# Performance work log

Hardware: AMD Instinct MI355X
Metric: run time of the kernel (lower is better)

The kernel has to match this reference:

```python
import jax, jax.numpy as jnp
import numpy as np

NUM_HEADS = 12
D = 768
HD = D // NUM_HEADS  # 64

def setup_inputs() -> dict:
    key = jax.random.key(0)
    ks = jax.random.split(key, 9)
    s = 0.02
    return {
        "x": jax.random.normal(ks[0], (4, 2048, D), dtype=jnp.float32),
        "QW_w": jax.random.normal(ks[1], (D, D), dtype=jnp.float32) * s,
        "QW_b": jax.random.normal(ks[2], (D,), dtype=jnp.float32) * s,
        "KW_w": jax.random.normal(ks[3], (D, D), dtype=jnp.float32) * s,
        "KW_b": jax.random.normal(ks[4], (D,), dtype=jnp.float32) * s,
        "VW_w": jax.random.normal(ks[5], (D, D), dtype=jnp.float32) * s,
        "VW_b": jax.random.normal(ks[6], (D,), dtype=jnp.float32) * s,
        "OW_w": jax.random.normal(ks[7], (D, D), dtype=jnp.float32) * s,
        "OW_b": jax.random.normal(ks[8], (D,), dtype=jnp.float32) * s,
    }

def reference(x, QW_w, QW_b, KW_w, KW_b, VW_w, VW_b, OW_w, OW_b):
    b, s, _ = x.shape
    # torch nn.Linear: y = x @ W.T + b
    def proj(w, bias):
        y = jnp.einsum('bsd,ed->bse', x, w) + bias
        return y.reshape(b, s, NUM_HEADS, HD).transpose(0, 2, 1, 3)  # [b,h,s,hd]
    q = proj(QW_w, QW_b)
    k = proj(KW_w, KW_b)
    v = proj(VW_w, VW_b)
    scores = jnp.einsum('bhqd,bhkd->bhqk', q, k) / jnp.sqrt(jnp.float32(HD))
    attn = jax.nn.softmax(scores, axis=-1)
    out = jnp.einsum('bhqk,bhkd->bhqd', attn, v)
    out = out.transpose(0, 2, 1, 3).reshape(b, s, NUM_HEADS * HD)
    return jnp.einsum('bsd,ed->bse', out, OW_w) + OW_b
```

## Files before the change

### kernel.cpp

```cpp
#include <hip/hip_runtime.h>
#include <hip/hip_bf16.h>

#define NH  12
#define HD  64
#define DIM 768
#define SEQ 2048
#define NB  4
#define MM  (NB*SEQ)
#define NKB (SEQ/64)

typedef short    v8s  __attribute__((ext_vector_type(8)));
typedef float    v4f  __attribute__((ext_vector_type(4)));
typedef float    v16f __attribute__((ext_vector_type(16)));
typedef unsigned v4u  __attribute__((ext_vector_type(4)));

#if __has_builtin(__builtin_amdgcn_exp2f)
#define EXP2(x) __builtin_amdgcn_exp2f(x)
#else
#define EXP2(x) __builtin_exp2f(x)
#endif

static __device__ __forceinline__ unsigned short f2b(float f) {
    unsigned int u = __float_as_uint(f);
    return (unsigned short)((u + 0x7FFFu + ((u >> 16) & 1u)) >> 16);
}
static __device__ __forceinline__ unsigned pk2bf(float lo, float hi) {
    return __builtin_amdgcn_perm(__float_as_uint(hi) + 0x8000u,
                                 __float_as_uint(lo) + 0x8000u, 0x07060302u);
}
static __device__ __forceinline__ void g2l16(const unsigned short* g, unsigned short* l) {
    __builtin_amdgcn_global_load_lds(
        (const __attribute__((address_space(1))) void*)g,
        (__attribute__((address_space(3))) void*)l, 16, 0, 0);
}

__global__ void cast_f32_bf16(const float* __restrict__ in,
                              unsigned short* __restrict__ out, int n4) {
    int i = blockIdx.x * blockDim.x + threadIdx.x;
    if (i < n4) {
        float4 v = reinterpret_cast<const float4*>(in)[i];
        ushort4 o;
        o.x = f2b(v.x); o.y = f2b(v.y); o.z = f2b(v.z); o.w = f2b(v.w);
        reinterpret_cast<ushort4*>(out)[i] = o;
    }
}

__global__ void cast4_f32_bf16(const float* __restrict__ i0, const float* __restrict__ i1,
                               const float* __restrict__ i2, const float* __restrict__ i3,
                               unsigned short* __restrict__ o0, unsigned short* __restrict__ o1,
                               unsigned short* __restrict__ o2, unsigned short* __restrict__ o3,
                               int n4) {
    int i = blockIdx.x * blockDim.x + threadIdx.x;
    if (i >= n4) return;
    const float* in; unsigned short* out;
    switch (blockIdx.y) {
        case 0: in = i0; out = o0; break;
        case 1: in = i1; out = o1; break;
        case 2: in = i2; out = o2; break;
        default: in = i3; out = o3; break;
    }
    float4 v = reinterpret_cast<const float4*>(in)[i];
    ushort4 o;
    o.x = f2b(v.x); o.y = f2b(v.y); o.z = f2b(v.z); o.w = f2b(v.w);
    reinterpret_cast<ushort4*>(out)[i] = o;
}

__global__ __launch_bounds__(256, 3) void gemm_qkv(
    const unsigned short* __restrict__ A,
    const unsigned short* __restrict__ Wq,
    const unsigned short* __restrict__ Wk,
    const unsigned short* __restrict__ Wv,
    const float* __restrict__ bq,
    const float* __restrict__ bk,
    const float* __restrict__ bvp,
    unsigned short* __restrict__ Qb,
    unsigned short* __restrict__ Kb,
    unsigned short* __restrict__ Vf)
{
    __shared__ __align__(16) unsigned short As[128 * 64];
    __shared__ __align__(16) unsigned short Bs[3][64 * 64];

    const int tid  = threadIdx.x;
    const int w    = tid >> 6, lane = tid & 63;
    const int quad = lane >> 4, l16 = lane & 15;
    const int wm   = w & 1,  wn = w >> 1;
    const int lane8 = lane >> 3, sc = lane & 7;
    const int m0   = blockIdx.x * 128;
    const int h    = blockIdx.y;
    const int n0   = h * 64;

    v4f acc[3][4][2];
    #pragma unroll
    for (int s = 0; s < 3; ++s)
        #pragma unroll
        for (int i = 0; i < 4; ++i)
            #pragma unroll
            for (int j = 0; j < 2; ++j)
                acc[s][i][j] = v4f{0.f, 0.f, 0.f, 0.f};

    for (int kb = 0; kb < DIM; kb += 64) {
        __syncthreads();
        #pragma unroll
        for (int t = 0; t < 4; ++t) {
            int r8 = w * 32 + t * 8;
            int r  = r8 + lane8;
            int gch = sc ^ (r & 7);
            g2l16(&A[(size_t)(m0 + r) * DIM + kb + gch * 8], &As[r8 * 64]);
        }
        #pragma unroll
        for (int u = 0; u < 6; ++u) {
            int G = w * 6 + u;
            int set = G >> 3, rg = G & 7;
            int row = rg * 8 + lane8;
            int gch = sc ^ (row & 7);
            const unsigned short* Wp = (set == 0) ? Wq : (set == 1) ? Wk : Wv;
            g2l16(&Wp[(size_t)(n0 + row) * DIM + kb + gch * 8], &Bs[set][rg * 8 * 64]);
        }
        __syncthreads();
        #pragma unroll
        for (int kk = 0; kk < 64; kk += 32) {
            int chb = kk >> 3;
            v8s a[4];
            #pragma unroll
            for (int i = 0; i < 4; ++i) {
                int m = wm * 64 + i * 16 + l16;
                a[i] = *reinterpret_cast<const v8s*>(
                    &As[m * 64 + (((chb + quad) ^ (m & 7)) << 3)]);
            }
            #pragma unroll
            for (int s = 0; s < 3; ++s) {
                v8s b[2];
                #pragma unroll
                for (int j = 0; j < 2; ++j) {
                    int n = wn * 32 + j * 16 + l16;
                    b[j] = *reinterpret_cast<const v8s*>(
                        &Bs[s][n * 64 + (((chb + quad) ^ (n & 7)) << 3)]);
                }
                #pragma unroll
                for (int i = 0; i < 4; ++i)
                    #pragma unroll
                    for (int j = 0; j < 2; ++j)
                        acc[s][i][j] = __builtin_amdgcn_mfma_f32_16x16x32_bf16(
                            a[i], b[j], acc[s][i][j], 0, 0, 0);
            }
        }
    }

    #pragma unroll
    for (int s = 0; s < 2; ++s) {
        unsigned short* out = s ? Kb : Qb;
        const float* bias   = s ? bk : bq;
        const float scale   = s ? 1.0f : 0.1803368801f;
        #pragma unroll
        for (int i = 0; i < 4; ++i) {
            #pragma unroll
            for (int j = 0; j < 2; ++j) {
                int hd = wn * 32 + j * 16 + l16;
                float bias_v = bias[n0 + hd];
                #pragma unroll
                for (int r = 0; r < 4; ++r) {
                    int gm = m0 + wm * 64 + i * 16 + quad * 4 + r;
                    int bb = gm >> 11, sq = gm & (SEQ - 1);
                    out[((size_t)(bb * NH + h) * SEQ + sq) * HD + hd] =
                        f2b((acc[s][i][j][r] + bias_v) * scale);
                }
            }
        }
    }
    #pragma unroll
    for (int i = 0; i < 4; ++i) {
        #pragma unroll
        for (int j = 0; j < 2; ++j) {
            int hd = wn * 32 + j * 16 + l16;
            int hb = hd >> 5, l31v = hd & 31;
            float bias_v = bvp[n0 + hd];
            int gm0 = m0 + wm * 64 + i * 16 + quad * 4;
            int bb = gm0 >> 11, sk = gm0 & (SEQ - 1);
            int kbi = sk >> 6;
            int halfv = quad >> 1, j0 = (quad & 1) * 4;
            ushort4 pkv;
            pkv.x = f2b(acc[2][i][j][0] + bias_v);
            pkv.y = f2b(acc[2][i][j][1] + bias_v);
            pkv.z = f2b(acc[2][i][j][2] + bias_v);
            pkv.w = f2b(acc[2][i][j][3] + bias_v);
            size_t frag = ((size_t)(bb * NH + h) * NKB + kbi) * 8 + hb * 4 + i;
            *reinterpret_cast<ushort4*>(
                &Vf[frag * 512 + (halfv * 32 + l31v) * 8 + j0]) = pkv;
        }
    }
}

__global__ __launch_bounds__(256) void gemm_o(
    const unsigned short* __restrict__ A,
    const unsigned short* __restrict__ W,
    const float* __restrict__ bias,
    float* __restrict__ out)
{
    __shared__ __align__(16) unsigned short As[128 * 64];
    __shared__ __align__(16) unsigned short Bs[128 * 64];

    const int tid  = threadIdx.x;
    const int w    = tid >> 6, lane = tid & 63;
    const int quad = lane >> 4, l16 = lane & 15;
    const int wm   = w & 1,  wn = w >> 1;
    const int lane8 = lane >> 3, sc = lane & 7;
    const int m0  = blockIdx.x * 128;
    const int n0l = blockIdx.y * 128;

    v4f acc[4][4];
    #pragma unroll
    for (int i = 0; i < 4; ++i)
        #pragma unroll
        for (int j = 0; j < 4; ++j)
            acc[i][j] = v4f{0.f, 0.f, 0.f, 0.f};

    for (int kb = 0; kb < DIM; kb += 64) {
        __syncthreads();
        #pragma unroll
        for (int t = 0; t < 4; ++t) {
            int r8 = w * 32 + t * 8;
            int r  = r8 + lane8;
            int gch = sc ^ (r & 7);
            g2l16(&A[(size_t)(m0  + r) * DIM + kb + gch * 8], &As[r8 * 64]);
            g2l16(&W[(size_t)(n0l + r) * DIM + kb + gch * 8], &Bs[r8 * 64]);
        }
        __syncthreads();
        #pragma unroll
        for (int kk = 0; kk < 64; kk += 32) {
            v8s a[4], b[4];
            int chb = kk >> 3;
            #pragma unroll
            for (int i = 0; i < 4; ++i) {
                int m = wm * 64 + i * 16 + l16;
                a[i] = *reinterpret_cast<const v8s*>(
                    &As[m * 64 + (((chb + quad) ^ (m & 7)) << 3)]);
                int n = wn * 64 + i * 16 + l16;
                b[i] = *reinterpret_cast<const v8s*>(
                    &Bs[n * 64 + (((chb + quad) ^ (n & 7)) << 3)]);
            }
            #pragma unroll
            for (int i = 0; i < 4; ++i)
                #pragma unroll
                for (int j = 0; j < 4; ++j)
                    acc[i][j] = __builtin_amdgcn_mfma_f32_16x16x32_bf16(a[i], b[j], acc[i][j], 0, 0, 0);
        }
    }

    #pragma unroll
    for (int i = 0; i < 4; ++i) {
        #pragma unroll
        for (int j = 0; j < 4; ++j) {
            int gn = n0l + wn * 64 + j * 16 + l16;
            float bias_v = bias[gn];
            #pragma unroll
            for (int r = 0; r < 4; ++r) {
                int gm = m0 + wm * 64 + i * 16 + quad * 4 + r;
                out[(size_t)gm * DIM + gn] = acc[i][j][r] + bias_v;
            }
        }
    }
}

__global__ __launch_bounds__(256, 3) void attn(
    const unsigned short* __restrict__ Q,
    const unsigned short* __restrict__ K,
    const unsigned short* __restrict__ Vf,
    unsigned short* __restrict__ ctx)
{
    __shared__ __align__(16) unsigned short Ks[2][64 * 64];

    const int tid  = threadIdx.x;
    const int w    = tid >> 6, lane = tid & 63;
    const int l31  = lane & 31, half = lane >> 5;
    const int lane8 = lane >> 3, sc = lane & 7;
    const int bh   = blockIdx.y;
    const int b    = bh / NH, h = bh % NH;
    const int q0   = blockIdx.x * 128 + w * 32;

    const unsigned short* Qp = Q  + ((size_t)bh * SEQ + q0) * HD;
    const unsigned short* Kp = K  + (size_t)bh * SEQ * HD;
    const unsigned short* Vh = Vf + (size_t)bh * NKB * 8 * 512 + lane * 8;

    v8s bq[4];
    #pragma unroll
    for (int c = 0; c < 4; ++c)
        bq[c] = *reinterpret_cast<const v8s*>(&Qp[l31 * HD + c * 16 + half * 8]);

    v8s va[2][4], vb[2][4];
    #pragma unroll
    for (int hb = 0; hb < 2; ++hb)
        #pragma unroll
        for (int c = 0; c < 4; ++c)
            va[hb][c] = *reinterpret_cast<const v8s*>(&Vh[(hb * 4 + c) * 512]);

    v16f o0, o1, Z;
    #pragma unroll
    for (int i = 0; i < 16; ++i) { o0[i] = 0.f; o1[i] = 0.f; Z[i] = 0.f; }
    float li = 0.f;

    const int rx = l31 & 7;
    int rdoff[4];
    #pragma unroll
    for (int c = 0; c < 4; ++c)
        rdoff[c] = l31 * 64 + (((c * 2 + half) ^ rx) << 3);

    #define STAGE_K(kb_, buf_)                                                       \
        do {                                                                         \
            _Pragma("unroll")                                                        \
            for (int t = 0; t < 2; ++t) {                                            \
                int r8  = (t * 4 + w) * 8;                                           \
                int row = r8 + lane8;                                                \
                int gch = sc ^ (row & 7);                                            \
                g2l16(&Kp[(size_t)((kb_) + row) * HD + gch * 8], &Ks[buf_][r8 * 64]);\
            }                                                                        \
        } while (0)

    #define TILE(IT, BUF, VCUR, VNEXT)                                               \
    {                                                                                \
        __syncthreads();                                                             \
        if ((IT) + 1 < NKB) {                                                        \
            STAGE_K(((IT) + 1) * 64, (BUF) ^ 1);                                     \
            const unsigned short* Vn = Vh + (size_t)((IT) + 1) * 8 * 512;            \
            _Pragma("unroll")                                                        \
            for (int hb = 0; hb < 2; ++hb)                                           \
                _Pragma("unroll")                                                    \
                for (int c = 0; c < 4; ++c)                                          \
                    VNEXT[hb][c] = *reinterpret_cast<const v8s*>(&Vn[(hb*4+c)*512]); \
        }                                                                            \
        v16f s0, s1;                                                                 \
        {                                                                            \
            v8s ka0 = *reinterpret_cast<const v8s*>(&Ks[BUF][rdoff[0]]);             \
            v8s ka1 = *reinterpret_cast<const v8s*>(&Ks[BUF][rdoff[0] + 2048]);      \
            s0 = __builtin_amdgcn_mfma_f32_32x32x16_bf16(ka0, bq[0], Z, 0, 0, 0);    \
            s1 = __builtin_amdgcn_mfma_f32_32x32x16_bf16(ka1, bq[0], Z, 0, 0, 0);    \
            _Pragma("unroll")                                                        \
            for (int c = 1; c < 4; ++c) {                                            \
                v8s k0 = *reinterpret_cast<const v8s*>(&Ks[BUF][rdoff[c]]);          \
                v8s k1 = *reinterpret_cast<const v8s*>(&Ks[BUF][rdoff[c] + 2048]);   \
                s0 = __builtin_amdgcn_mfma_f32_32x32x16_bf16(k0, bq[c], s0, 0, 0, 0);\
                s1 = __builtin_amdgcn_mfma_f32_32x32x16_bf16(k1, bq[c], s1, 0, 0, 0);\
            }                                                                        \
        }                                                                            \
        unsigned pk[8][2];                                                           \
        _Pragma("unroll")                                                            \
        for (int g = 0; g < 4; ++g) {                                                \
            float e0 = EXP2(s0[4*g+0]), e1 = EXP2(s0[4*g+1]);                        \
            float e2 = EXP2(s0[4*g+2]), e3 = EXP2(s0[4*g+3]);                        \
            li += (e0 + e1) + (e2 + e3);                                             \
            pk[g][0] = pk2bf(e0, e1);                                                \
            pk[g][1] = pk2bf(e2, e3);                                                \
            float f0 = EXP2(s1[4*g+0]), f1 = EXP2(s1[4*g+1]);                        \
            float f2 = EXP2(s1[4*g+2]), f3 = EXP2(s1[4*g+3]);                        \
            li += (f0 + f1) + (f2 + f3);                                             \
            pk[4+g][0] = pk2bf(f0, f1);                                              \
            pk[4+g][1] = pk2bf(f2, f3);                                              \
        }                                                                            \
        _Pragma("unroll")                                                            \
        for (int cp = 0; cp < 4; ++cp) {                                             \
            unsigned a0 = pk[2*cp][0],   a1 = pk[2*cp][1];                           \
            unsigned b0 = pk[2*cp+1][0], b1 = pk[2*cp+1][1];                         \
            unsigned u0 = half ? a0 : b0;                                            \
            unsigned u1 = half ? a1 : b1;                                            \
            unsigned x0 = __shfl_xor(u0, 32);                                        \
            unsigned x1 = __shfl_xor(u1, 32);                                        \
            v4u fw;                                                                  \
            fw.x = half ? x0 : a0;                                                   \
            fw.y = half ? x1 : a1;                                                   \
            fw.z = half ? b0 : x0;                                                   \
            fw.w = half ? b1 : x1;                                                   \
            v8s pf = __builtin_bit_cast(v8s, fw);                                    \
            o0 = __builtin_amdgcn_mfma_f32_32x32x16_bf16(VCUR[0][cp], pf, o0, 0,0,0);\
            o1 = __builtin_amdgcn_mfma_f32_32x32x16_bf16(VCUR[1][cp], pf, o1, 0,0,0);\
        }                                                                            \
    }

    STAGE_K(0, 0);

    for (int it = 0; it < NKB; it += 2) {
        TILE(it,     0, va, vb)
        TILE(it + 1, 1, vb, va)
    }
    #undef TILE
    #undef STAGE_K

    float inv = 1.0f / (li + __shfl_xor(li, 32));

    const int q = q0 + l31;
    size_t base = ((size_t)(b * SEQ + q)) * DIM + h * HD;
    #pragma unroll
    for (int g = 0; g < 4; ++g) {
        int hd0 = 8 * g + 4 * half;
        uint2 u0, u1;
        u0.x = pk2bf(o0[4*g+0] * inv, o0[4*g+1] * inv);
        u0.y = pk2bf(o0[4*g+2] * inv, o0[4*g+3] * inv);
        u1.x = pk2bf(o1[4*g+0] * inv, o1[4*g+1] * inv);
        u1.y = pk2bf(o1[4*g+2] * inv, o1[4*g+3] * inv);
        *reinterpret_cast<uint2*>(&ctx[base + hd0])      = u0;
        *reinterpret_cast<uint2*>(&ctx[base + 32 + hd0]) = u1;
    }
}

extern "C" void kernel_launch(void* const* d_in, const int* in_sizes, int n_in,
                              void* d_out, int out_size, void* d_ws, size_t ws_size,
                              hipStream_t stream) {
    const float* x  = (const float*)d_in[0];
    const float* qw = (const float*)d_in[1]; const float* qb = (const float*)d_in[2];
    const float* kw = (const float*)d_in[3]; const float* kb = (const float*)d_in[4];
    const float* vw = (const float*)d_in[5]; const float* vb = (const float*)d_in[6];
    const float* ow = (const float*)d_in[7]; const float* ob = (const float*)d_in[8];
    float* out = (float*)d_out;

    char* ws = (char*)d_ws;
    size_t off = 0;
    auto alloc = [&](size_t bytes) -> unsigned short* {
        unsigned short* p = (unsigned short*)(ws + off);
        off += (bytes + 255) & ~(size_t)255;
        return p;
    };
    const size_t XB = (size_t)MM * DIM * 2;
    const size_t WB = (size_t)DIM * DIM * 2;
    const size_t QB = (size_t)NB * NH * SEQ * HD * 2;

    unsigned short* xb  = alloc(XB);
    unsigned short* wqb = alloc(WB);
    unsigned short* wkb = alloc(WB);
    unsigned short* wvb = alloc(WB);
    unsigned short* wob = alloc(WB);
    unsigned short* Qb  = alloc(QB);
    unsigned short* Kb  = alloc(QB);
    unsigned short* Vfb = alloc(QB);
    unsigned short* ctx = alloc(XB);

    const int n4x = MM * DIM / 4;
    const int n4w = DIM * DIM / 4;
    cast_f32_bf16<<<(n4x + 255) / 256, 256, 0, stream>>>(x, xb, n4x);
    cast4_f32_bf16<<<dim3((n4w + 255) / 256, 4), 256, 0, stream>>>(
        qw, kw, vw, ow, wqb, wkb, wvb, wob, n4w);

    gemm_qkv<<<dim3(MM / 128, NH), 256, 0, stream>>>(
        xb, wqb, wkb, wvb, qb, kb, vb, Qb, Kb, Vfb);

    attn<<<dim3(SEQ / 128, NB * NH), 256, 0, stream>>>(Qb, Kb, Vfb, ctx);

    gemm_o<<<dim3(MM / 128, DIM / 128), 256, 0, stream>>>(ctx, wob, ob, out);
}
```

Measured before the change: 228.7 us.

## Shrink output GEMM N-tile and single-buffer V fragments in attention

```diff
diff --git a/kernel.cpp b/kernel.cpp
--- a/kernel.cpp
+++ b/kernel.cpp
@@ -190,14 +190,14 @@
     }
 }
 
-__global__ __launch_bounds__(256) void gemm_o(
+__global__ __launch_bounds__(256, 3) void gemm_o(
     const unsigned short* __restrict__ A,
     const unsigned short* __restrict__ W,
     const float* __restrict__ bias,
     float* __restrict__ out)
 {
     __shared__ __align__(16) unsigned short As[128 * 64];
-    __shared__ __align__(16) unsigned short Bs[128 * 64];
+    __shared__ __align__(16) unsigned short Bs[64 * 64];
 
     const int tid  = threadIdx.x;
     const int w    = tid >> 6, lane = tid & 63;
@@ -205,13 +205,13 @@
     const int wm   = w & 1,  wn = w >> 1;
     const int lane8 = lane >> 3, sc = lane & 7;
     const int m0  = blockIdx.x * 128;
-    const int n0l = blockIdx.y * 128;
-
-    v4f acc[4][4];
+    const int n0l = blockIdx.y * 64;
+
+    v4f acc[4][2];
     #pragma unroll
     for (int i = 0; i < 4; ++i)
         #pragma unroll
-        for (int j = 0; j < 4; ++j)
+        for (int j = 0; j < 2; ++j)
             acc[i][j] = v4f{0.f, 0.f, 0.f, 0.f};
 
     for (int kb = 0; kb < DIM; kb += 64) {
@@ -221,27 +221,36 @@
             int r8 = w * 32 + t * 8;
             int r  = r8 + lane8;
             int gch = sc ^ (r & 7);
-            g2l16(&A[(size_t)(m0  + r) * DIM + kb + gch * 8], &As[r8 * 64]);
+            g2l16(&A[(size_t)(m0 + r) * DIM + kb + gch * 8], &As[r8 * 64]);
+        }
+        #pragma unroll
+        for (int t = 0; t < 2; ++t) {
+            int r8 = (w * 2 + t) * 8;
+            int r  = r8 + lane8;
+            int gch = sc ^ (r & 7);
             g2l16(&W[(size_t)(n0l + r) * DIM + kb + gch * 8], &Bs[r8 * 64]);
         }
         __syncthreads();
         #pragma unroll
         for (int kk = 0; kk < 64; kk += 32) {
-            v8s a[4], b[4];
+            v8s a[4], b[2];
             int chb = kk >> 3;
             #pragma unroll
             for (int i = 0; i < 4; ++i) {
                 int m = wm * 64 + i * 16 + l16;
                 a[i] = *reinterpret_cast<const v8s*>(
                     &As[m * 64 + (((chb + quad) ^ (m & 7)) << 3)]);
-                int n = wn * 64 + i * 16 + l16;
-                b[i] = *reinterpret_cast<const v8s*>(
+            }
+            #pragma unroll
+            for (int j = 0; j < 2; ++j) {
+                int n = wn * 32 + j * 16 + l16;
+                b[j] = *reinterpret_cast<const v8s*>(
                     &Bs[n * 64 + (((chb + quad) ^ (n & 7)) << 3)]);
             }
             #pragma unroll
             for (int i = 0; i < 4; ++i)
                 #pragma unroll
-                for (int j = 0; j < 4; ++j)
+                for (int j = 0; j < 2; ++j)
                     acc[i][j] = __builtin_amdgcn_mfma_f32_16x16x32_bf16(a[i], b[j], acc[i][j], 0, 0, 0);
         }
     }
@@ -249,8 +258,8 @@
     #pragma unroll
     for (int i = 0; i < 4; ++i) {
         #pragma unroll
-        for (int j = 0; j < 4; ++j) {
-            int gn = n0l + wn * 64 + j * 16 + l16;
+        for (int j = 0; j < 2; ++j) {
+            int gn = n0l + wn * 32 + j * 16 + l16;
             float bias_v = bias[gn];
             #pragma unroll
             for (int r = 0; r < 4; ++r) {
@@ -286,7 +295,7 @@
     for (int c = 0; c < 4; ++c)
         bq[c] = *reinterpret_cast<const v8s*>(&Qp[l31 * HD + c * 16 + half * 8]);
 
-    v8s va[2][4], vb[2][4];
+    v8s va[2][4];
     #pragma unroll
     for (int hb = 0; hb < 2; ++hb)
         #pragma unroll
@@ -315,72 +324,70 @@
             }                                                                        \
         } while (0)
 
-    #define TILE(IT, BUF, VCUR, VNEXT)                                               \
-    {                                                                                \
-        __syncthreads();                                                             \
-        if ((IT) + 1 < NKB) {                                                        \
-            STAGE_K(((IT) + 1) * 64, (BUF) ^ 1);                                     \
-            const unsigned short* Vn = Vh + (size_t)((IT) + 1) * 8 * 512;            \
-            _Pragma("unroll")                                                        \
-            for (int hb = 0; hb < 2; ++hb)                                           \
-                _Pragma("unroll")                                                    \
-                for (int c = 0; c < 4; ++c)                                          \
-                    VNEXT[hb][c] = *reinterpret_cast<const v8s*>(&Vn[(hb*4+c)*512]); \
-        }                                                                            \
-        v16f s0, s1;                                                                 \
-        {                                                                            \
-            v8s ka0 = *reinterpret_cast<const v8s*>(&Ks[BUF][rdoff[0]]);             \
-            v8s ka1 = *reinterpret_cast<const v8s*>(&Ks[BUF][rdoff[0] + 2048]);      \
-            s0 = __builtin_amdgcn_mfma_f32_32x32x16_bf16(ka0, bq[0], Z, 0, 0, 0);    \
-            s1 = __builtin_amdgcn_mfma_f32_32x32x16_bf16(ka1, bq[0], Z, 0, 0, 0);    \
-            _Pragma("unroll")                                                        \
-            for (int c = 1; c < 4; ++c) {                                            \
-                v8s k0 = *reinterpret_cast<const v8s*>(&Ks[BUF][rdoff[c]]);          \
-                v8s k1 = *reinterpret_cast<const v8s*>(&Ks[BUF][rdoff[c] + 2048]);   \
-                s0 = __builtin_amdgcn_mfma_f32_32x32x16_bf16(k0, bq[c], s0, 0, 0, 0);\
-                s1 = __builtin_amdgcn_mfma_f32_32x32x16_bf16(k1, bq[c], s1, 0, 0, 0);\
-            }                                                                        \
-        }                                                                            \
-        unsigned pk[8][2];                                                           \
-        _Pragma("unroll")                                                            \
-        for (int g = 0; g < 4; ++g) {                                                \
-            float e0 = EXP2(s0[4*g+0]), e1 = EXP2(s0[4*g+1]);                        \
-            float e2 = EXP2(s0[4*g+2]), e3 = EXP2(s0[4*g+3]);                        \
-            li += (e0 + e1) + (e2 + e3);                                             \
-            pk[g][0] = pk2bf(e0, e1);                                                \
-            pk[g][1] = pk2bf(e2, e3);                                                \
-            float f0 = EXP2(s1[4*g+0]), f1 = EXP2(s1[4*g+1]);                        \
-            float f2 = EXP2(s1[4*g+2]), f3 = EXP2(s1[4*g+3]);                        \
-            li += (f0 + f1) + (f2 + f3);                                             \
-            pk[4+g][0] = pk2bf(f0, f1);                                              \
-            pk[4+g][1] = pk2bf(f2, f3);                                              \
-        }                                                                            \
-        _Pragma("unroll")                                                            \
-        for (int cp = 0; cp < 4; ++cp) {                                             \
-            unsigned a0 = pk[2*cp][0],   a1 = pk[2*cp][1];                           \
-            unsigned b0 = pk[2*cp+1][0], b1 = pk[2*cp+1][1];                         \
-            unsigned u0 = half ? a0 : b0;                                            \
-            unsigned u1 = half ? a1 : b1;                                            \
-            unsigned x0 = __shfl_xor(u0, 32);                                        \
-            unsigned x1 = __shfl_xor(u1, 32);                                        \
-            v4u fw;                                                                  \
-            fw.x = half ? x0 : a0;                                                   \
-            fw.y = half ? x1 : a1;                                                   \
-            fw.z = half ? b0 : x0;                                                   \
-            fw.w = half ? b1 : x1;                                                   \
-            v8s pf = __builtin_bit_cast(v8s, fw);                                    \
-            o0 = __builtin_amdgcn_mfma_f32_32x32x16_bf16(VCUR[0][cp], pf, o0, 0,0,0);\
-            o1 = __builtin_amdgcn_mfma_f32_32x32x16_bf16(VCUR[1][cp], pf, o1, 0,0,0);\
-        }                                                                            \
-    }
-
     STAGE_K(0, 0);
 
-    for (int it = 0; it < NKB; it += 2) {
-        TILE(it,     0, va, vb)
-        TILE(it + 1, 1, vb, va)
-    }
-    #undef TILE
+    for (int it = 0; it < NKB; ++it) {
+        const int buf = it & 1;
+        __syncthreads();
+        if (it + 1 < NKB) STAGE_K((it + 1) * 64, buf ^ 1);
+
+        v16f s0, s1;
+        {
+            v8s ka00 = *reinterpret_cast<const v8s*>(&Ks[buf][rdoff[0]]);
+            v8s ka10 = *reinterpret_cast<const v8s*>(&Ks[buf][rdoff[0] + 2048]);
+            s0 = __builtin_amdgcn_mfma_f32_32x32x16_bf16(ka00, bq[0], Z, 0, 0, 0);
+            s1 = __builtin_amdgcn_mfma_f32_32x32x16_bf16(ka10, bq[0], Z, 0, 0, 0);
+            #pragma unroll
+            for (int c = 1; c < 4; ++c) {
+                v8s k0 = *reinterpret_cast<const v8s*>(&Ks[buf][rdoff[c]]);
+                v8s k1 = *reinterpret_cast<const v8s*>(&Ks[buf][rdoff[c] + 2048]);
+                s0 = __builtin_amdgcn_mfma_f32_32x32x16_bf16(k0, bq[c], s0, 0, 0, 0);
+                s1 = __builtin_amdgcn_mfma_f32_32x32x16_bf16(k1, bq[c], s1, 0, 0, 0);
+            }
+        }
+
+        unsigned pk[8][2];
+        #pragma unroll
+        for (int g = 0; g < 4; ++g) {
+            float e0 = EXP2(s0[4*g+0]), e1 = EXP2(s0[4*g+1]);
+            float e2 = EXP2(s0[4*g+2]), e3 = EXP2(s0[4*g+3]);
+            li += (e0 + e1) + (e2 + e3);
+            pk[g][0] = pk2bf(e0, e1);
+            pk[g][1] = pk2bf(e2, e3);
+            float f0 = EXP2(s1[4*g+0]), f1 = EXP2(s1[4*g+1]);
+            float f2 = EXP2(s1[4*g+2]), f3 = EXP2(s1[4*g+3]);
+            li += (f0 + f1) + (f2 + f3);
+            pk[4+g][0] = pk2bf(f0, f1);
+            pk[4+g][1] = pk2bf(f2, f3);
+        }
+
+        #pragma unroll
+        for (int cp = 0; cp < 4; ++cp) {
+            unsigned a0 = pk[2*cp][0],   a1 = pk[2*cp][1];
+            unsigned b0 = pk[2*cp+1][0], b1 = pk[2*cp+1][1];
+            unsigned u0 = half ? a0 : b0;
+            unsigned u1 = half ? a1 : b1;
+            unsigned x0 = __shfl_xor(u0, 32);
+            unsigned x1 = __shfl_xor(u1, 32);
+            v4u fw;
+            fw.x = half ? x0 : a0;
+            fw.y = half ? x1 : a1;
+            fw.z = half ? b0 : x0;
+            fw.w = half ? b1 : x1;
+            v8s pf = __builtin_bit_cast(v8s, fw);
+            o0 = __builtin_amdgcn_mfma_f32_32x32x16_bf16(va[0][cp], pf, o0, 0, 0, 0);
+            o1 = __builtin_amdgcn_mfma_f32_32x32x16_bf16(va[1][cp], pf, o1, 0, 0, 0);
+        }
+
+        if (it + 1 < NKB) {
+            const unsigned short* Vn = Vh + (size_t)(it + 1) * 8 * 512;
+            #pragma unroll
+            for (int hb = 0; hb < 2; ++hb)
+                #pragma unroll
+                for (int c = 0; c < 4; ++c)
+                    va[hb][c] = *reinterpret_cast<const v8s*>(&Vn[(hb * 4 + c) * 512]);
+        }
+    }
     #undef STAGE_K
 
     float inv = 1.0f / (li + __shfl_xor(li, 32));
@@ -442,5 +449,5 @@
 
     attn<<<dim3(SEQ / 128, NB * NH), 256, 0, stream>>>(Qb, Kb, Vfb, ctx);
 
-    gemm_o<<<dim3(MM / 128, DIM / 128), 256, 0, stream>>>(ctx, wob, ob, out);
-}
+    gemm_o<<<dim3(MM / 128, DIM / 64), 256, 0, stream>>>(ctx, wob, ob, out);
+}
```

Measured after the change: 208.7 us. 8.7% less time.
